# Performance work log

Hardware: AMD Instinct MI355X
Metric: run time of the kernel (lower is better)

## Reference

```python
import jax, jax.numpy as jnp
import numpy as np

ALPHA = 0.1  # LeakyReLU negative slope
F_OUT = 128

def _leaky(x):
    return jnp.where(x >= 0, x, ALPHA * x)

def setup_inputs() -> dict:
    key = jax.random.key(0)
    ks = jax.random.split(key, 12)
    B, N, F_IN = 4, 4096, 128
    q = jax.random.normal(ks[0], (B, N, F_IN), jnp.float32)
    k = jax.random.normal(ks[1], (B, N, F_IN), jnp.float32)
    v = jax.random.normal(ks[2], (B, N, F_IN), jnp.float32)
    adj = jax.random.randint(ks[3], (B, N, N), 0, 2, jnp.int32)
    s = 1.0 / np.sqrt(F_IN)
    Wq_w = jax.random.uniform(ks[4], (F_OUT, F_IN), jnp.float32, -s, s)
    Wq_b = jax.random.uniform(ks[5], (F_OUT,), jnp.float32, -s, s)
    Wk_w = jax.random.uniform(ks[6], (F_OUT, F_IN), jnp.float32, -s, s)
    Wk_b = jax.random.uniform(ks[7], (F_OUT,), jnp.float32, -s, s)
    Wv_w = jax.random.uniform(ks[8], (F_OUT, F_IN), jnp.float32, -s, s)
    Wv_b = jax.random.uniform(ks[9], (F_OUT,), jnp.float32, -s, s)
    # xavier_uniform with gain=1.414 on (2F,1)
    lim = 1.414 * np.sqrt(6.0 / (2 * F_OUT + 1))
    a = jax.random.uniform(ks[10], (2 * F_OUT, 1), jnp.float32, -lim, lim)
    so = 1.0 / np.sqrt(F_OUT)
    Wo_w = jax.random.uniform(ks[11], (F_OUT, F_OUT), jnp.float32, -so, so)
    return {"q": q, "k": k, "v": v, "adj": adj, "Wq_w": Wq_w, "Wq_b": Wq_b,
            "Wk_w": Wk_w, "Wk_b": Wk_b, "Wv_w": Wv_w, "Wv_b": Wv_b,
            "a": a, "Wo_w": Wo_w}

def reference(q, k, v, adj, Wq_w, Wq_b, Wk_w, Wk_b, Wv_w, Wv_b, a, Wo_w):
    qp = q @ Wq_w.T + Wq_b                      # (B,N,F)
    kp = k @ Wk_w.T + Wk_b
    vp = v @ Wv_w.T + Wv_b
    Wh1 = qp @ a[:F_OUT]                        # (B,N,1)
    Wh2 = kp @ a[F_OUT:]                        # (B,N,1)
    e = _leaky(Wh1 + jnp.swapaxes(Wh2, 1, 2))   # (B,N,N)
    e = jnp.where(adj > 0, e, jnp.float32(-1e9))
    att = jax.nn.softmax(e, axis=-1)
    h = jnp.einsum('bnm,bmf->bnf', att, vp)     # (B,N,F)
    return _leaky(h @ Wo_w.T)
```

## Files before the change

### kernel.cpp

```cpp
#include <hip/hip_runtime.h>


constexpr int B = 4, N = 4096, F = 128;
constexpr int BN = B * N;
constexpr int BK = 64;
constexpr int SPLITS = 4;
constexpr int JC = N / SPLITS;
constexpr int NIT = JC / BK;
#define ALPHA 0.1f

using float4v = __attribute__((ext_vector_type(4))) float;
using short8 = __attribute__((ext_vector_type(8))) short;
typedef unsigned long long ull;

__device__ __forceinline__ float leaky(float x) { return x >= 0.f ? x : ALPHA * x; }
__device__ __forceinline__ unsigned short f2bf(float x) {
    unsigned u = __float_as_uint(x);
    u = (u + 0x7FFFu + ((u >> 16) & 1u)) >> 16;
    return (unsigned short)u;
}
__device__ __forceinline__ unsigned pack_bf2(float lo, float hi) {
    unsigned a = __float_as_uint(lo), b2 = __float_as_uint(hi);
    a = a + 0x7FFFu + ((a >> 16) & 1u);
    b2 = b2 + 0x7FFFu + ((b2 >> 16) & 1u);
    return __builtin_amdgcn_perm(b2, a, 0x07060302u);
}

__global__ __launch_bounds__(256) void k_pack(const int* __restrict__ adj,
                                              ull* __restrict__ pack) {
    const long long GROUPS = (long long)B * N * N / 256;
    int t = threadIdx.x;
    int lane = t & 63;
    long long gw = ((long long)blockIdx.x * 256 + t) >> 6;
    long long nw = ((long long)gridDim.x * 256) >> 6;
    for (long long g = gw; g < GROUPS; g += nw) {
        long long base = g * 256;
        ull m0 = __ballot(adj[base + lane] != 0);
        ull m1 = __ballot(adj[base + 64 + lane] != 0);
        ull m2 = __ballot(adj[base + 128 + lane] != 0);
        ull m3 = __ballot(adj[base + 192 + lane] != 0);
        if (lane < 4) {
            ull w = (lane == 0) ? m0 : (lane == 1) ? m1 : (lane == 2) ? m2 : m3;
            pack[g * 4 + lane] = w;
        }
    }
}

__global__ void k_prep(const float* __restrict__ Wq_w, const float* __restrict__ Wq_b,
                       const float* __restrict__ Wk_w, const float* __restrict__ Wk_b,
                       const float* __restrict__ a, float* __restrict__ c1,
                       float* __restrict__ c2, float* __restrict__ d12) {
    __shared__ float as[2 * F];
    __shared__ float red[2 * F];
    int t = threadIdx.x;
    as[t] = a[t];
    __syncthreads();
    int f = t & 127;
    const float* W = (t < F) ? Wq_w : Wk_w;
    const float* ao = (t < F) ? as : as + F;
    float s = 0.f;
#pragma unroll 8
    for (int o = 0; o < F; o++) s = fmaf(W[o * F + f], ao[o], s);
    if (t < F) c1[f] = s; else c2[f] = s;
    red[t] = (t < F) ? Wq_b[f] * as[f] : Wk_b[f] * as[F + f];
    __syncthreads();
    for (int st = 64; st > 0; st >>= 1) {
        if (f < st) red[t] += red[t + st];
        __syncthreads();
    }
    if (t == 0) d12[0] = red[0];
    if (t == F) d12[1] = red[F];
}

__global__ void k_wh(const float* __restrict__ q, const float* __restrict__ k,
                     const float* __restrict__ c1, const float* __restrict__ c2,
                     const float* __restrict__ d12,
                     float* __restrict__ Wh1, float* __restrict__ Wh2) {
    __shared__ float c1s[F], c2s[F];
    int t = threadIdx.x;
    if (t < F) c1s[t] = c1[t]; else c2s[t - F] = c2[t - F];
    __syncthreads();
    int row = blockIdx.x * 8 + (t >> 5);
    int lane = t & 31;
    float4 q4 = reinterpret_cast<const float4*>(q)[row * 32 + lane];
    float4 k4 = reinterpret_cast<const float4*>(k)[row * 32 + lane];
    float s1 = q4.x * c1s[lane * 4 + 0] + q4.y * c1s[lane * 4 + 1] +
               q4.z * c1s[lane * 4 + 2] + q4.w * c1s[lane * 4 + 3];
    float s2 = k4.x * c2s[lane * 4 + 0] + k4.y * c2s[lane * 4 + 1] +
               k4.z * c2s[lane * 4 + 2] + k4.w * c2s[lane * 4 + 3];
    for (int m = 16; m > 0; m >>= 1) { s1 += __shfl_xor(s1, m); s2 += __shfl_xor(s2, m); }
    if (lane == 0) { Wh1[row] = s1 + d12[0]; Wh2[row] = s2 + d12[1]; }
}

__global__ void k_max2(const float* __restrict__ Wh2, float* __restrict__ M2) {
    int b = blockIdx.x, t = threadIdx.x;
    float m = -1e30f;
    for (int i = t; i < N; i += 256) m = fmaxf(m, Wh2[b * N + i]);
    __shared__ float red[256];
    red[t] = m;
    __syncthreads();
    for (int s = 128; s > 0; s >>= 1) { if (t < s) red[t] = fmaxf(red[t], red[t + s]); __syncthreads(); }
    if (t == 0) M2[b] = red[0];
}

__global__ void k_tab(const float* __restrict__ Wh1, const float* __restrict__ Wh2,
                      const float* __restrict__ M2,
                      float* __restrict__ P1, float* __restrict__ Q1,
                      float* __restrict__ P2, float* __restrict__ Q2) {
    int i = blockIdx.x * 256 + threadIdx.x;
    int b = i >> 12;
    float w1 = Wh1[i], w2 = Wh2[i];
    float mi = leaky(w1 + M2[b]);
    P1[i] = __expf(w1 - mi);
    Q1[i] = __expf(ALPHA * w1 - mi);
    P2[i] = __expf(w2);
    Q2[i] = __expf(ALPHA * w2);
}

__global__ __launch_bounds__(256) void k_vp(const float* __restrict__ v,
                                            const float* __restrict__ Wv_w,
                                            const float* __restrict__ Wv_b,
                                            unsigned short* __restrict__ vpT) {
    __shared__ float vs[32][F];
    __shared__ float Ws[F][129];
    __shared__ unsigned short ts[F][40];
    int t = threadIdx.x;
    int row0g = blockIdx.x * 32;
    int b = row0g >> 12;
    int row0 = row0g & (N - 1);
    {
        const float4* src = reinterpret_cast<const float4*>(v + row0g * F);
        float4* dst = reinterpret_cast<float4*>(&vs[0][0]);
#pragma unroll
        for (int u = 0; u < 4; u++) dst[u * 256 + t] = src[u * 256 + t];
    }
    {
        const float4* src = reinterpret_cast<const float4*>(Wv_w);
#pragma unroll
        for (int u = 0; u < 16; u++) {
            int unit = u * 256 + t;
            int r = unit >> 5, s = unit & 31;
            float4 val = src[unit];
            Ws[r][s * 4 + 0] = val.x; Ws[r][s * 4 + 1] = val.y;
            Ws[r][s * 4 + 2] = val.z; Ws[r][s * 4 + 3] = val.w;
        }
    }
    int f = t & 127, g = t >> 7;
    float bias = Wv_b[f];
    __syncthreads();
    float acc[16];
#pragma unroll
    for (int r = 0; r < 16; r++) acc[r] = bias;
    for (int kk = 0; kk < F; kk++) {
        float wk = Ws[f][kk];
#pragma unroll
        for (int r = 0; r < 16; r++) acc[r] = fmaf(vs[g * 16 + r][kk], wk, acc[r]);
    }
#pragma unroll
    for (int r = 0; r < 16; r++) ts[f][g * 16 + r] = f2bf(acc[r]);
    __syncthreads();
    int fr = t >> 1, hseg = t & 1;
    uint4 d0 = *reinterpret_cast<uint4*>(&ts[fr][hseg * 16]);
    uint4 d1 = *reinterpret_cast<uint4*>(&ts[fr][hseg * 16 + 8]);
    unsigned short* dst = vpT + ((size_t)(b * F + fr) * N + row0 + hseg * 16);
    *reinterpret_cast<uint4*>(dst) = d0;
    *reinterpret_cast<uint4*>(dst + 8) = d1;
}

__global__ __launch_bounds__(256, 3) void k_attn(
    const unsigned short* __restrict__ vpT, const ull* __restrict__ pack,
    const float* __restrict__ Wh1, const float* __restrict__ P1, const float* __restrict__ Q1,
    const float* __restrict__ P2, const float* __restrict__ Q2, const float* __restrict__ Wh2,
    float* __restrict__ h_part, float* __restrict__ den_part) {
    __shared__ __align__(16) unsigned short bs[2][F][72];
    __shared__ __align__(16) float sP2[JC], sQ2[JC], sW2[JC];
    int t = threadIdx.x;
    int idx = blockIdx.x;
    int split = idx & 3;
    int tile = (idx >> 2) & 63;
    int b = idx >> 8;
    int i0 = tile * 64;
    int jb0 = split * JC;
    int widx = t >> 6, lane = t & 63, m = lane & 15, q = lane >> 4;

    {
        reinterpret_cast<float4*>(sP2)[t] = reinterpret_cast<const float4*>(P2 + b * N + jb0)[t];
        reinterpret_cast<float4*>(sQ2)[t] = reinterpret_cast<const float4*>(Q2 + b * N + jb0)[t];
        reinterpret_cast<float4*>(sW2)[t] = reinterpret_cast<const float4*>(Wh2 + b * N + jb0)[t];
    }

    int gi = b * N + i0 + widx * 16 + m;
    float p1 = P1[gi], q1 = Q1[gi], t1 = -Wh1[gi];
    const ull* pk = pack + (size_t)gi * (N / 64) + jb0 / 64;
    const unsigned short* vb = vpT + (size_t)b * F * N + jb0;

    uint4 sreg[4];
    auto load_stage = [&](int it) {
#pragma unroll
        for (int u = 0; u < 4; u++) {
            int unit = u * 256 + t;
            int r = unit >> 3, s = unit & 7;
            sreg[u] = *reinterpret_cast<const uint4*>(vb + (size_t)r * N + it * BK + s * 8);
        }
    };
    auto write_stage = [&](int pb) {
#pragma unroll
        for (int u = 0; u < 4; u++) {
            int unit = u * 256 + t;
            int r = unit >> 3, s = unit & 7;
            *reinterpret_cast<uint4*>(&bs[pb][r][s * 8]) = sreg[u];
        }
    };

    float4v acc[8];
#pragma unroll
    for (int nt = 0; nt < 8; nt++) acc[nt] = (float4v){0.f, 0.f, 0.f, 0.f};
    float den = 0.f;

    auto gen_af = [&](unsigned bt, const float4& x2a, const float4& x2b,
                      const float4& p2a, const float4& p2b, const float4& q2a,
                      const float4& q2b, float& dn) -> short8 {
        float w0 = (bt & 1u)   ? ((x2a.x >= t1) ? p1 * p2a.x : q1 * q2a.x) : 0.f;
        float w1 = (bt & 2u)   ? ((x2a.y >= t1) ? p1 * p2a.y : q1 * q2a.y) : 0.f;
        float w2 = (bt & 4u)   ? ((x2a.z >= t1) ? p1 * p2a.z : q1 * q2a.z) : 0.f;
        float w3 = (bt & 8u)   ? ((x2a.w >= t1) ? p1 * p2a.w : q1 * q2a.w) : 0.f;
        float w4 = (bt & 16u)  ? ((x2b.x >= t1) ? p1 * p2b.x : q1 * q2b.x) : 0.f;
        float w5 = (bt & 32u)  ? ((x2b.y >= t1) ? p1 * p2b.y : q1 * q2b.y) : 0.f;
        float w6 = (bt & 64u)  ? ((x2b.z >= t1) ? p1 * p2b.z : q1 * q2b.z) : 0.f;
        float w7 = (bt & 128u) ? ((x2b.w >= t1) ? p1 * p2b.w : q1 * q2b.w) : 0.f;
        dn += ((w0 + w1) + (w2 + w3)) + ((w4 + w5) + (w6 + w7));
        union { short8 s; uint4 u; } r;
        r.u.x = pack_bf2(w0, w1); r.u.y = pack_bf2(w2, w3);
        r.u.z = pack_bf2(w4, w5); r.u.w = pack_bf2(w6, w7);
        return r.s;
    };

    auto body = [&](int it, int pb, ull pw, ull& pwn) {
        if (it + 1 < NIT) {
            load_stage(it + 1);
            pwn = pk[it + 1];
        }
#pragma unroll
        for (int kh = 0; kh < 2; kh++) {
            int jl = it * BK + kh * 32 + q * 8;
            float4 x2a = *reinterpret_cast<const float4*>(&sW2[jl]);
            float4 x2b = *reinterpret_cast<const float4*>(&sW2[jl + 4]);
            float4 p2a = *reinterpret_cast<const float4*>(&sP2[jl]);
            float4 p2b = *reinterpret_cast<const float4*>(&sP2[jl + 4]);
            float4 q2a = *reinterpret_cast<const float4*>(&sQ2[jl]);
            float4 q2b = *reinterpret_cast<const float4*>(&sQ2[jl + 4]);
            unsigned bt = ((unsigned)(pw >> (kh * 32)) >> (q * 8)) & 0xFFu;
            short8 af = gen_af(bt, x2a, x2b, p2a, p2b, q2a, q2b, den);
#pragma unroll
            for (int nt = 0; nt < 8; nt++) {
                short8 bf = *reinterpret_cast<const short8*>(&bs[pb][nt * 16 + m][kh * 32 + q * 8]);
                acc[nt] = __builtin_amdgcn_mfma_f32_16x16x32_bf16(af, bf, acc[nt], 0, 0, 0);
            }
        }
        if (it + 1 < NIT) write_stage(pb ^ 1);
        __syncthreads();
    };

    ull pwA, pwB;
    load_stage(0);
    pwA = pk[0];
    write_stage(0);
    __syncthreads();

#pragma unroll 1
    for (int ith = 0; ith < NIT / 2; ith++) {
        body(ith * 2 + 0, 0, pwA, pwB);
        body(ith * 2 + 1, 1, pwB, pwA);
    }

    den += __shfl_xor(den, 16);
    den += __shfl_xor(den, 32);
    float* dp = den_part + (size_t)split * BN;
    if (q == 0) dp[gi] = den;
    float* hp = h_part + (size_t)split * BN * F;
    int orow = b * N + i0 + widx * 16 + q * 4;
#pragma unroll
    for (int nt = 0; nt < 8; nt++)
#pragma unroll
        for (int r = 0; r < 4; r++)
            hp[(size_t)(orow + r) * F + nt * 16 + m] = acc[nt][r];
}

__global__ __launch_bounds__(256) void k_out(const float* __restrict__ h_part,
                                             const float* __restrict__ den_part,
                                             const float* __restrict__ Wo_w,
                                             float* __restrict__ out) {
    __shared__ float hs[32][F];
    __shared__ float Ws[F][129];
    int t = threadIdx.x;
    int row0 = blockIdx.x * 32;
    {
        const float4* src = reinterpret_cast<const float4*>(Wo_w);
#pragma unroll
        for (int u = 0; u < 16; u++) {
            int unit = u * 256 + t;
            int r = unit >> 5, s = unit & 31;
            float4 val = src[unit];
            Ws[r][s * 4 + 0] = val.x; Ws[r][s * 4 + 1] = val.y;
            Ws[r][s * 4 + 2] = val.z; Ws[r][s * 4 + 3] = val.w;
        }
    }
#pragma unroll
    for (int u = 0; u < 4; u++) {
        int unit = u * 256 + t;
        int r = unit >> 5, s = unit & 31;
        size_t off = (size_t)(row0 + r) * F + s * 4;
        float4 h0 = *reinterpret_cast<const float4*>(h_part + off);
        float4 h1 = *reinterpret_cast<const float4*>(h_part + (size_t)BN * F + off);
        float4 h2 = *reinterpret_cast<const float4*>(h_part + (size_t)2 * BN * F + off);
        float4 h3 = *reinterpret_cast<const float4*>(h_part + (size_t)3 * BN * F + off);
        float dsum = den_part[row0 + r] + den_part[BN + row0 + r] +
                     den_part[2 * BN + row0 + r] + den_part[3 * BN + row0 + r];
        float inv = 1.f / dsum;
        hs[r][s * 4 + 0] = (h0.x + h1.x + h2.x + h3.x) * inv;
        hs[r][s * 4 + 1] = (h0.y + h1.y + h2.y + h3.y) * inv;
        hs[r][s * 4 + 2] = (h0.z + h1.z + h2.z + h3.z) * inv;
        hs[r][s * 4 + 3] = (h0.w + h1.w + h2.w + h3.w) * inv;
    }
    __syncthreads();
    int f = t & 127, g = t >> 7;
    float acc[16];
#pragma unroll
    for (int r = 0; r < 16; r++) acc[r] = 0.f;
    for (int kk = 0; kk < F; kk++) {
        float wk = Ws[f][kk];
#pragma unroll
        for (int r = 0; r < 16; r++) acc[r] = fmaf(hs[g * 16 + r][kk], wk, acc[r]);
    }
#pragma unroll
    for (int r = 0; r < 16; r++) out[(size_t)(row0 + g * 16 + r) * F + f] = leaky(acc[r]);
}

extern "C" void kernel_launch(void* const* d_in, const int* in_sizes, int n_in,
                              void* d_out, int out_size, void* d_ws, size_t ws_size,
                              hipStream_t stream) {
    const float* q    = (const float*)d_in[0];
    const float* k    = (const float*)d_in[1];
    const float* v    = (const float*)d_in[2];
    const int*   adj  = (const int*)d_in[3];
    const float* Wq_w = (const float*)d_in[4];
    const float* Wq_b = (const float*)d_in[5];
    const float* Wk_w = (const float*)d_in[6];
    const float* Wk_b = (const float*)d_in[7];
    const float* Wv_w = (const float*)d_in[8];
    const float* Wv_b = (const float*)d_in[9];
    const float* a    = (const float*)d_in[10];
    const float* Wo_w = (const float*)d_in[11];
    float* out = (float*)d_out;
    float* ws = (float*)d_ws;

    unsigned short* vpT = (unsigned short*)ws;
    float* h_part   = ws + BN * F / 2;
    float* den_part = h_part + (size_t)SPLITS * BN * F;
    float* Wh1 = den_part + SPLITS * BN;
    float* Wh2 = Wh1 + BN;
    float* P1  = Wh2 + BN;
    float* Q1  = P1 + BN;
    float* P2  = Q1 + BN;
    float* Q2  = P2 + BN;
    float* c1  = Q2 + BN;
    float* c2  = c1 + F;
    float* d12 = c2 + F;
    float* M2  = d12 + 2;
    size_t off = (size_t)((M2 + B) - ws);
    off = (off + 1) & ~(size_t)1;
    ull* pack = (ull*)(ws + off);

    k_pack<<<2048, 256, 0, stream>>>(adj, pack);
    k_prep<<<1, 256, 0, stream>>>(Wq_w, Wq_b, Wk_w, Wk_b, a, c1, c2, d12);
    k_wh<<<BN / 8, 256, 0, stream>>>(q, k, c1, c2, d12, Wh1, Wh2);
    k_max2<<<B, 256, 0, stream>>>(Wh2, M2);
    k_tab<<<BN / 256, 256, 0, stream>>>(Wh1, Wh2, M2, P1, Q1, P2, Q2);
    k_vp<<<BN / 32, 256, 0, stream>>>(v, Wv_w, Wv_b, vpT);
    k_attn<<<B * 64 * SPLITS, 256, 0, stream>>>(vpT, pack, Wh1, P1, Q1, P2, Q2, Wh2,
                                                h_part, den_part);
    k_out<<<BN / 32, 256, 0, stream>>>(h_part, den_part, Wo_w, out);
}
```

Before: 538.7 us.

## Double attention row tile per block and transpose adjacency bitmask for coalesced loads

The attention kernel now processes 128 query rows per block instead of 64, with each wave handling two 16-row MFMA A fragments that share the same staged V tile. This halves V staging traffic and LDS fills per unit of work. A new kernel transposes the packed adjacency bitmask so each iteration's mask words are read contiguously across lanes. The cost is double the accumulator registers, occupancy lowered from 3 to 2 blocks per CU, half as many blocks (512), and an extra transpose pass over the mask.

```diff
diff --git a/kernel.cpp b/kernel.cpp
--- a/kernel.cpp
+++ b/kernel.cpp
@@ -46,6 +46,28 @@
     }
 }
 
+__global__ __launch_bounds__(256) void k_ptrans(const ull* __restrict__ pack,
+                                                ull* __restrict__ packT) {
+    __shared__ ull tile[64][65];
+    int t = threadIdx.x;
+    int blk = blockIdx.x;
+    int b = blk >> 6;
+    int i0 = (blk & 63) * 64;
+#pragma unroll
+    for (int u = 0; u < 16; u++) {
+        int unit = u * 256 + t;
+        tile[unit >> 6][unit & 63] =
+            pack[((size_t)b * N + i0 + (unit >> 6)) * 64 + (unit & 63)];
+    }
+    __syncthreads();
+#pragma unroll
+    for (int u = 0; u < 16; u++) {
+        int unit = u * 256 + t;
+        packT[((size_t)b * 64 + (unit >> 6)) * N + i0 + (unit & 63)] =
+            tile[unit & 63][unit >> 6];
+    }
+}
+
 __global__ void k_prep(const float* __restrict__ Wq_w, const float* __restrict__ Wq_b,
                        const float* __restrict__ Wk_w, const float* __restrict__ Wk_b,
                        const float* __restrict__ a, float* __restrict__ c1,
@@ -167,8 +189,8 @@
     *reinterpret_cast<uint4*>(dst + 8) = d1;
 }
 
-__global__ __launch_bounds__(256, 3) void k_attn(
-    const unsigned short* __restrict__ vpT, const ull* __restrict__ pack,
+__global__ __launch_bounds__(256, 2) void k_attn(
+    const unsigned short* __restrict__ vpT, const ull* __restrict__ packT,
     const float* __restrict__ Wh1, const float* __restrict__ P1, const float* __restrict__ Q1,
     const float* __restrict__ P2, const float* __restrict__ Q2, const float* __restrict__ Wh2,
     float* __restrict__ h_part, float* __restrict__ den_part) {
@@ -177,9 +199,9 @@
     int t = threadIdx.x;
     int idx = blockIdx.x;
     int split = idx & 3;
-    int tile = (idx >> 2) & 63;
-    int b = idx >> 8;
-    int i0 = tile * 64;
+    int tile = (idx >> 2) & 31;
+    int b = idx >> 7;
+    int i0 = tile * 128;
     int jb0 = split * JC;
     int widx = t >> 6, lane = t & 63, m = lane & 15, q = lane >> 4;
 
@@ -189,9 +211,12 @@
         reinterpret_cast<float4*>(sW2)[t] = reinterpret_cast<const float4*>(Wh2 + b * N + jb0)[t];
     }
 
-    int gi = b * N + i0 + widx * 16 + m;
-    float p1 = P1[gi], q1 = Q1[gi], t1 = -Wh1[gi];
-    const ull* pk = pack + (size_t)gi * (N / 64) + jb0 / 64;
+    int gi0 = b * N + i0 + widx * 32 + m;
+    int gi1 = gi0 + 16;
+    float p1a = P1[gi0], q1a = Q1[gi0], t1a = -Wh1[gi0];
+    float p1b = P1[gi1], q1b = Q1[gi1], t1b = -Wh1[gi1];
+
+    const ull* pt = packT + ((size_t)b * 64 + (size_t)split * 16) * N + i0 + widx * 32 + m;
     const unsigned short* vb = vpT + (size_t)b * F * N + jb0;
 
     uint4 sreg[4];
@@ -212,14 +237,17 @@
         }
     };
 
-    float4v acc[8];
-#pragma unroll
-    for (int nt = 0; nt < 8; nt++) acc[nt] = (float4v){0.f, 0.f, 0.f, 0.f};
-    float den = 0.f;
+    float4v acc0[8], acc1[8];
+#pragma unroll
+    for (int nt = 0; nt < 8; nt++) {
+        acc0[nt] = (float4v){0.f, 0.f, 0.f, 0.f};
+        acc1[nt] = (float4v){0.f, 0.f, 0.f, 0.f};
+    }
+    float den0 = 0.f, den1 = 0.f;
 
     auto gen_af = [&](unsigned bt, const float4& x2a, const float4& x2b,
                       const float4& p2a, const float4& p2b, const float4& q2a,
-                      const float4& q2b, float& dn) -> short8 {
+                      const float4& q2b, float p1, float q1, float t1, float& dn) -> short8 {
         float w0 = (bt & 1u)   ? ((x2a.x >= t1) ? p1 * p2a.x : q1 * q2a.x) : 0.f;
         float w1 = (bt & 2u)   ? ((x2a.y >= t1) ? p1 * p2a.y : q1 * q2a.y) : 0.f;
         float w2 = (bt & 4u)   ? ((x2a.z >= t1) ? p1 * p2a.z : q1 * q2a.z) : 0.f;
@@ -235,10 +263,11 @@
         return r.s;
     };
 
-    auto body = [&](int it, int pb, ull pw, ull& pwn) {
+    auto body = [&](int it, int pb, ull pw0, ull pw1, ull& nx0, ull& nx1) {
         if (it + 1 < NIT) {
             load_stage(it + 1);
-            pwn = pk[it + 1];
+            nx0 = pt[(size_t)(it + 1) * N];
+            nx1 = pt[(size_t)(it + 1) * N + 16];
         }
 #pragma unroll
         for (int kh = 0; kh < 2; kh++) {
@@ -249,41 +278,47 @@
             float4 p2b = *reinterpret_cast<const float4*>(&sP2[jl + 4]);
             float4 q2a = *reinterpret_cast<const float4*>(&sQ2[jl]);
             float4 q2b = *reinterpret_cast<const float4*>(&sQ2[jl + 4]);
-            unsigned bt = ((unsigned)(pw >> (kh * 32)) >> (q * 8)) & 0xFFu;
-            short8 af = gen_af(bt, x2a, x2b, p2a, p2b, q2a, q2b, den);
+            unsigned bt0 = ((unsigned)(pw0 >> (kh * 32)) >> (q * 8)) & 0xFFu;
+            unsigned bt1 = ((unsigned)(pw1 >> (kh * 32)) >> (q * 8)) & 0xFFu;
+            short8 af0 = gen_af(bt0, x2a, x2b, p2a, p2b, q2a, q2b, p1a, q1a, t1a, den0);
+            short8 af1 = gen_af(bt1, x2a, x2b, p2a, p2b, q2a, q2b, p1b, q1b, t1b, den1);
 #pragma unroll
             for (int nt = 0; nt < 8; nt++) {
                 short8 bf = *reinterpret_cast<const short8*>(&bs[pb][nt * 16 + m][kh * 32 + q * 8]);
-                acc[nt] = __builtin_amdgcn_mfma_f32_16x16x32_bf16(af, bf, acc[nt], 0, 0, 0);
+                acc0[nt] = __builtin_amdgcn_mfma_f32_16x16x32_bf16(af0, bf, acc0[nt], 0, 0, 0);
+                acc1[nt] = __builtin_amdgcn_mfma_f32_16x16x32_bf16(af1, bf, acc1[nt], 0, 0, 0);
             }
         }
         if (it + 1 < NIT) write_stage(pb ^ 1);
         __syncthreads();
     };
 
-    ull pwA, pwB;
+    ull pwA0, pwA1, pwB0, pwB1;
     load_stage(0);
-    pwA = pk[0];
+    pwA0 = pt[0];
+    pwA1 = pt[16];
     write_stage(0);
     __syncthreads();
 
 #pragma unroll 1
     for (int ith = 0; ith < NIT / 2; ith++) {
-        body(ith * 2 + 0, 0, pwA, pwB);
-        body(ith * 2 + 1, 1, pwB, pwA);
-    }
-
-    den += __shfl_xor(den, 16);
-    den += __shfl_xor(den, 32);
+        body(ith * 2 + 0, 0, pwA0, pwA1, pwB0, pwB1);
+        body(ith * 2 + 1, 1, pwB0, pwB1, pwA0, pwA1);
+    }
+
+    den0 += __shfl_xor(den0, 16); den0 += __shfl_xor(den0, 32);
+    den1 += __shfl_xor(den1, 16); den1 += __shfl_xor(den1, 32);
     float* dp = den_part + (size_t)split * BN;
-    if (q == 0) dp[gi] = den;
+    if (q == 0) { dp[gi0] = den0; dp[gi1] = den1; }
     float* hp = h_part + (size_t)split * BN * F;
-    int orow = b * N + i0 + widx * 16 + q * 4;
+    int orow = b * N + i0 + widx * 32 + q * 4;
 #pragma unroll
     for (int nt = 0; nt < 8; nt++)
 #pragma unroll
-        for (int r = 0; r < 4; r++)
-            hp[(size_t)(orow + r) * F + nt * 16 + m] = acc[nt][r];
+        for (int r = 0; r < 4; r++) {
+            hp[(size_t)(orow + r) * F + nt * 16 + m] = acc0[nt][r];
+            hp[(size_t)(orow + 16 + r) * F + nt * 16 + m] = acc1[nt][r];
+        }
 }
 
 __global__ __launch_bounds__(256) void k_out(const float* __restrict__ h_part,
@@ -368,16 +403,18 @@
     float* d12 = c2 + F;
     float* M2  = d12 + 2;
     size_t off = (size_t)((M2 + B) - ws);
-    off = (off + 1) & ~(size_t)1;
-    ull* pack = (ull*)(ws + off);
+    off = (off + 3) & ~(size_t)3;
+    ull* pack  = (ull*)(ws + off);
+    ull* packT = pack + (size_t)BN * (N / 64);
 
     k_pack<<<2048, 256, 0, stream>>>(adj, pack);
+    k_ptrans<<<B * 64, 256, 0, stream>>>(pack, packT);
     k_prep<<<1, 256, 0, stream>>>(Wq_w, Wq_b, Wk_w, Wk_b, a, c1, c2, d12);
     k_wh<<<BN / 8, 256, 0, stream>>>(q, k, c1, c2, d12, Wh1, Wh2);
     k_max2<<<B, 256, 0, stream>>>(Wh2, M2);
     k_tab<<<BN / 256, 256, 0, stream>>>(Wh1, Wh2, M2, P1, Q1, P2, Q2);
     k_vp<<<BN / 32, 256, 0, stream>>>(v, Wv_w, Wv_b, vpT);
-    k_attn<<<B * 64 * SPLITS, 256, 0, stream>>>(vpT, pack, Wh1, P1, Q1, P2, Q2, Wh2,
+    k_attn<<<B * 32 * SPLITS, 256, 0, stream>>>(vpT, packT, Wh1, P1, Q1, P2, Q2, Wh2,
                                                 h_part, den_part);
     k_out<<<BN / 32, 256, 0, stream>>>(h_part, den_part, Wo_w, out);
 }
```

New measurement: 523.0 us. 2.9% less time.
